# Optimization experiments

Measured on AMD Instinct MI355X. Metric: run time of the kernel, lower is better.

Reference implementation:

```python
import jax, jax.numpy as jnp
import numpy as np

N = 100000
E = 1600000
NUM_GRAPHS = 128
IN_C = 11
HID = 128


def setup_inputs() -> dict:
    key = jax.random.key(0)
    ks = jax.random.split(key, 16)
    x = jax.random.normal(ks[0], (N, IN_C), dtype=jnp.float32)
    edge_index = jax.random.randint(ks[1], (2, E), 0, N, dtype=jnp.int64)
    batch = jnp.sort(jax.random.randint(ks[2], (N,), 0, NUM_GRAPHS, dtype=jnp.int64))
    s_in = 1.0 / np.sqrt(IN_C)
    s_h = 1.0 / np.sqrt(HID)
    params = {
        'W1': jax.random.normal(ks[3], (IN_C, HID), jnp.float32) * s_in,
        'b1': jnp.zeros((HID,), jnp.float32),
        'W2': jax.random.normal(ks[4], (HID, HID), jnp.float32) * s_h,
        'b2': jnp.zeros((HID,), jnp.float32),
        'W4': jax.random.normal(ks[5], (HID, HID), jnp.float32) * s_h,
        'b4': jnp.zeros((HID,), jnp.float32),
        'Wd1': jax.random.normal(ks[6], (HID, HID), jnp.float32) * s_h,
        'bd1': jnp.zeros((HID,), jnp.float32),
        'Wd2': jax.random.normal(ks[7], (HID, HID), jnp.float32) * s_h,
        'bd2': jnp.zeros((HID,), jnp.float32),
        'Wo': jax.random.normal(ks[8], (HID, 1), jnp.float32) * s_h,
        'bo': jnp.zeros((1,), jnp.float32),
    }
    return {'x': x, 'edge_index': edge_index, 'batch': batch, **params}


def _gcn_norm(edge_index, n_nodes):
    # add self loops, compute symmetric normalization (PyG GCNConv defaults)
    loop = jnp.arange(n_nodes, dtype=edge_index.dtype)
    row = jnp.concatenate([edge_index[0], loop])
    col = jnp.concatenate([edge_index[1], loop])
    deg = jax.ops.segment_sum(jnp.ones_like(col, dtype=jnp.float32), col,
                              num_segments=n_nodes)
    dinv = jnp.where(deg > 0, jax.lax.rsqrt(deg), 0.0)
    norm = dinv[row] * dinv[col]  # [E+N]
    return row, col, norm


def _gcn_conv(h, row, col, norm, W, b, n_nodes):
    h = h @ W  # dense lin first (PyG order)
    msg = norm[:, None] * h[row]            # gather + normalize
    out = jax.ops.segment_sum(msg, col, num_segments=n_nodes)  # scatter-add
    return out + b


def reference(x, edge_index, batch, W1, b1, W2, b2, W4, b4,
              Wd1, bd1, Wd2, bd2, Wo, bo):
    n = x.shape[0]
    row, col, norm = _gcn_norm(edge_index, n)
    # dropout is identity in eval mode
    h = jax.nn.relu(_gcn_conv(x, row, col, norm, W1, b1, n))
    h = jax.nn.relu(_gcn_conv(h, row, col, norm, W2, b2, n))
    h = _gcn_conv(h, row, col, norm, W4, b4, n)
    # global_mean_pool over batch ids
    sums = jax.ops.segment_sum(h, batch, num_segments=NUM_GRAPHS)
    cnts = jax.ops.segment_sum(jnp.ones((n,), jnp.float32), batch,
                               num_segments=NUM_GRAPHS)
    g = sums / jnp.maximum(cnts, 1.0)[:, None]  # [NUM_GRAPHS, HID]
    g = jax.nn.relu(g @ Wd1 + bd1)
    g = jax.nn.relu(g @ Wd2 + bd2)
    return g @ Wo + bo  # [NUM_GRAPHS, 1]
```

## Files before the change

### kernel.cpp

```cpp
#include <hip/hip_runtime.h>
#include <hip/hip_fp16.h>

#define HIDDEN 128
#define BSHIFT 8
#define BMASK 255
#define CHUNK 4096
#define BCAP 6144

typedef _Float16 h8 __attribute__((ext_vector_type(8)));
typedef float f4x __attribute__((ext_vector_type(4)));

__global__ __launch_bounds__(256) void fill_bin(const int* __restrict__ row,
                                                const int* __restrict__ col,
                                                int* __restrict__ bcnt,
                                                int2* __restrict__ ptmp, int E) {
    __shared__ int cnt[512], start[512], place[512], gbase[512];
    __shared__ int ssum[256];
    __shared__ int2 stage[CHUNK];
    int t = threadIdx.x;
    int e0 = blockIdx.x * CHUNK;
    int e1 = min(e0 + CHUNK, E);
    cnt[t] = 0; cnt[t + 256] = 0;
    __syncthreads();
    for (int e = e0 + t; e < e1; e += 256)
        atomicAdd(&cnt[col[e] >> BSHIFT], 1);
    __syncthreads();
    int s2 = cnt[2 * t] + cnt[2 * t + 1];
    ssum[t] = s2;
    __syncthreads();
    for (int d = 1; d < 256; d <<= 1) {
        int v = (t >= d) ? ssum[t - d] : 0;
        __syncthreads();
        ssum[t] += v;
        __syncthreads();
    }
    int excl = ssum[t] - s2;
    start[2 * t] = excl;
    start[2 * t + 1] = excl + cnt[2 * t];
    place[2 * t] = excl;
    place[2 * t + 1] = excl + cnt[2 * t];
    __syncthreads();
    for (int e = e0 + t; e < e1; e += 256) {
        int c = col[e], r = row[e];
        int slot = atomicAdd(&place[c >> BSHIFT], 1);
        stage[slot] = make_int2(r, c);
    }
    {
        int c0 = cnt[t], c1 = cnt[t + 256];
        if (c0 > 0) gbase[t] = atomicAdd(&bcnt[t], c0);
        if (c1 > 0) gbase[t + 256] = atomicAdd(&bcnt[t + 256], c1);
    }
    __syncthreads();
    int n = e1 - e0;
    for (int i = t; i < n; i += 256) {
        int2 p = stage[i];
        int b = p.y >> BSHIFT;
        ptmp[(size_t)b * BCAP + gbase[b] + (i - start[b])] = p;
    }
}

__global__ __launch_bounds__(512) void scan_buckets(const int* __restrict__ bcnt,
                                                    int* __restrict__ bbase, int NB) {
    __shared__ int s[512];
    int t = threadIdx.x;
    int v0 = (t < NB) ? bcnt[t] : 0;
    s[t] = v0;
    __syncthreads();
    for (int d = 1; d < 512; d <<= 1) {
        int v = (t >= d) ? s[t - d] : 0;
        __syncthreads();
        s[t] += v;
        __syncthreads();
    }
    bbase[t] = s[t] - v0;
}

__global__ __launch_bounds__(256) void fill_scatter(const int2* __restrict__ ptmp,
                                                    const int* __restrict__ bcnt,
                                                    const int* __restrict__ bbase,
                                                    const float* __restrict__ x,
                                                    int* __restrict__ offsets,
                                                    float* __restrict__ dinv,
                                                    int* __restrict__ sorted_r,
                                                    __half* __restrict__ xp,
                                                    int N, int E) {
    __shared__ int2 stage[BCAP];
    __shared__ int cnt[256], loff[256], cur[256];
    int b = blockIdx.x, t = threadIdx.x;
    int m = bcnt[b];
    int base = bbase[b];
    int nbase = b << BSHIFT;
    cnt[t] = 0;
    __syncthreads();
    for (int i = t; i < m; i += 256) {
        int2 p = ptmp[(size_t)b * BCAP + i];
        stage[i] = p;
        atomicAdd(&cnt[p.y & BMASK], 1);
    }
    __syncthreads();
    int my = cnt[t];
    loff[t] = my;
    __syncthreads();
    for (int d = 1; d < 256; d <<= 1) {
        int v = (t >= d) ? loff[t - d] : 0;
        __syncthreads();
        loff[t] += v;
        __syncthreads();
    }
    int excl = loff[t] - my;
    cur[t] = excl;
    int node = nbase + t;
    float dv = rsqrtf((float)(my + 1));
    if (node < N) {
        offsets[node] = base + excl;
        dinv[node] = dv;
        __half hrow[16];
#pragma unroll
        for (int c = 0; c < 11; ++c)
            hrow[c] = __float2half(x[(size_t)node * 11 + c] * dv);
#pragma unroll
        for (int c = 11; c < 16; ++c) hrow[c] = __float2half(0.f);
        *(uint4*)(xp + (size_t)node * 16)     = *(uint4*)hrow;
        *(uint4*)(xp + (size_t)node * 16 + 8) = *(uint4*)(hrow + 8);
    }
    if (b == gridDim.x - 1 && t == 0) offsets[N] = E;
    __syncthreads();
    for (int i = t; i < m; i += 256) {
        int2 p = stage[i];
        int slot = atomicAdd(&cur[p.y & BMASK], 1);
        sorted_r[base + slot] = p.x;
    }
}

__global__ __launch_bounds__(256) void agg16_fused(const __half* __restrict__ xp,
                                                   const float* __restrict__ W1,
                                                   const int* __restrict__ offsets,
                                                   const int* __restrict__ sorted_r,
                                                   const float* __restrict__ dinv,
                                                   __half* __restrict__ out, int N) {
    __shared__ float W1s[11 * 128];
    __shared__ float arow[4][16];
    int t = threadIdx.x;
    for (int q = t; q < 11 * 128; q += 256) W1s[q] = W1[q];
    int wv = t >> 6, lane = t & 63;
    int c = blockIdx.x * 4 + wv;
    bool valid = c < N;
    int g = lane >> 3, cp = lane & 7;
    const __half2* xp2 = (const __half2*)xp;
    float ax = 0.f, ay = 0.f;
    if (valid) {
        int beg = offsets[c], end = offsets[c + 1];
        if (g == 0) {
            float2 v = __half22float2(xp2[(size_t)c * 8 + cp]);
            ax = v.x; ay = v.y;
        }
        int i = beg;
        for (; i + 16 <= end; i += 16) {
            int r0 = sorted_r[i + g];
            int r1 = sorted_r[i + g + 8];
            float2 v0 = __half22float2(xp2[(size_t)r0 * 8 + cp]);
            float2 v1 = __half22float2(xp2[(size_t)r1 * 8 + cp]);
            ax += v0.x + v1.x; ay += v0.y + v1.y;
        }
        if (i < end) {
            int last = end - 1;
            int i0 = i + g, i1 = i + g + 8;
            int r0 = sorted_r[min(i0, last)];
            int r1 = sorted_r[min(i1, last)];
            float2 v0 = __half22float2(xp2[(size_t)r0 * 8 + cp]);
            float2 v1 = __half22float2(xp2[(size_t)r1 * 8 + cp]);
            if (i0 <= last) { ax += v0.x; ay += v0.y; }
            if (i1 <= last) { ax += v1.x; ay += v1.y; }
        }
    }
    ax += __shfl_xor(ax, 32); ay += __shfl_xor(ay, 32);
    ax += __shfl_xor(ax, 16); ay += __shfl_xor(ay, 16);
    ax += __shfl_xor(ax, 8);  ay += __shfl_xor(ay, 8);
    if (valid && lane < 8) {
        float dc = dinv[c];
        arow[wv][cp * 2]     = ax * dc;
        arow[wv][cp * 2 + 1] = ay * dc;
    }
    __syncthreads();
    int j = t & 127, half = t >> 7;
#pragma unroll
    for (int nn = 0; nn < 2; ++nn) {
        int n = half * 2 + nn;
        int node = blockIdx.x * 4 + n;
        if (node < N) {
            float acc = 0.f;
#pragma unroll
            for (int cc = 0; cc < 11; ++cc) acc += arow[n][cc] * W1s[cc * 128 + j];
            out[(size_t)node * HIDDEN + j] = __float2half(acc);
        }
    }
}

__global__ __launch_bounds__(256) void pack_w(const float* __restrict__ W,
                                              const float* __restrict__ bias,
                                              __half* __restrict__ packed) {
    int q = blockIdx.x * 256 + threadIdx.x;
    if (q < 2048) {
        int s = q >> 9, rem = q & 511, ct = rem >> 6, l = rem & 63;
        int b = l >> 4, n = l & 15;
        __half hi8[8], lo8[8];
#pragma unroll
        for (int i = 0; i < 8; ++i) {
            float w = W[(s * 32 + b * 8 + i) * HIDDEN + ct * 16 + n];
            __half h = __float2half(w);
            hi8[i] = h;
            lo8[i] = __float2half(w - __half2float(h));
        }
        *(uint4*)(packed + (size_t)q * 8)         = *(uint4*)hi8;
        *(uint4*)(packed + 16384 + (size_t)q * 8) = *(uint4*)lo8;
    }
    if (q < 128) packed[32768 + q] = __float2half(bias[q]);
}

__global__ __launch_bounds__(256, 2) void gemm_mfma(const __half* __restrict__ H,
                                                    const __half* __restrict__ packed,
                                                    const float* __restrict__ dinv,
                                                    __half* __restrict__ out,
                                                    int N, int ngroups) {
    int l = threadIdx.x & 63, wv = threadIdx.x >> 6;
    int cthalf = wv & 1;
    int n16 = l & 15, koct = l >> 4;
    h8 whi[4][4], wlo[4][4];
#pragma unroll
    for (int s = 0; s < 4; ++s)
#pragma unroll
        for (int mt = 0; mt < 4; ++mt) {
            int ct = cthalf * 4 + mt;
            whi[s][mt] = *(const h8*)(packed + (size_t)((s * 8 + ct) * 64 + l) * 8);
            wlo[s][mt] = *(const h8*)(packed + 16384 + (size_t)((s * 8 + ct) * 64 + l) * 8);
        }
    h8 biasf[4];
    const __half* bias_h = packed + 32768;
#pragma unroll
    for (int s = 0; s < 4; ++s)
        biasf[s] = *(const h8*)(bias_h + s * 32 + koct * 8);

    for (int g = blockIdx.x * 2 + (wv >> 1); g < ngroups; g += gridDim.x * 2) {
        int node = g * 16 + n16;
        bool ok = node < N;
        f4x acc[4];
#pragma unroll
        for (int mt = 0; mt < 4; ++mt) acc[mt] = (f4x){0.f, 0.f, 0.f, 0.f};
#pragma unroll
        for (int s = 0; s < 4; ++s) {
            uint4 bv = make_uint4(0u, 0u, 0u, 0u);
            if (ok) bv = *(const uint4*)(H + (size_t)node * HIDDEN + s * 32 + koct * 8);
            __half2* bh2 = (__half2*)&bv;
            const __half2* bb = (const __half2*)&biasf[s];
#pragma unroll
            for (int p = 0; p < 4; ++p) {
                float2 f  = __half22float2(bh2[p]);
                float2 bf = __half22float2(bb[p]);
                bh2[p] = __floats2half2_rn(fmaxf(f.x + bf.x, 0.f), fmaxf(f.y + bf.y, 0.f));
            }
            h8 bfrag = *(h8*)&bv;
#pragma unroll
            for (int mt = 0; mt < 4; ++mt) {
                acc[mt] = __builtin_amdgcn_mfma_f32_16x16x32_f16(whi[s][mt], bfrag, acc[mt], 0, 0, 0);
                acc[mt] = __builtin_amdgcn_mfma_f32_16x16x32_f16(wlo[s][mt], bfrag, acc[mt], 0, 0, 0);
            }
        }
        if (ok) {
            float dv = dinv[node];
#pragma unroll
            for (int mt = 0; mt < 4; ++mt) {
                int ch = (cthalf * 4 + mt) * 16 + koct * 4;
                __half2 h01 = __floats2half2_rn(acc[mt][0] * dv, acc[mt][1] * dv);
                __half2 h23 = __floats2half2_rn(acc[mt][2] * dv, acc[mt][3] * dv);
                uint2 o;
                o.x = *(unsigned int*)&h01; o.y = *(unsigned int*)&h23;
                *(uint2*)(out + (size_t)node * HIDDEN + ch) = o;
            }
        }
    }
}

__global__ __launch_bounds__(256) void agg128h(const __half* __restrict__ src,
                                               __half* __restrict__ dst,
                                               const int* __restrict__ offsets,
                                               const int* __restrict__ sorted_r,
                                               const float* __restrict__ dinv, int N) {
    int wid  = (blockIdx.x * 256 + threadIdx.x) >> 6;
    int lane = threadIdx.x & 63;
    if (wid >= N) return;
    int c = wid;
    int beg = offsets[c], end = offsets[c + 1];
    int g = lane >> 4, sub = lane & 15;
    const uint4* hp = (const uint4*)src;
    float a0=0.f,a1=0.f,a2=0.f,a3=0.f,a4=0.f,a5=0.f,a6=0.f,a7=0.f;

    auto accum = [&](uint4 u) {
        __half2 p0 = *(__half2*)&u.x, p1 = *(__half2*)&u.y;
        __half2 p2 = *(__half2*)&u.z, p3 = *(__half2*)&u.w;
        float2 f0 = __half22float2(p0), f1 = __half22float2(p1);
        float2 f2 = __half22float2(p2), f3 = __half22float2(p3);
        a0 += f0.x; a1 += f0.y; a2 += f1.x; a3 += f1.y;
        a4 += f2.x; a5 += f2.y; a6 += f3.x; a7 += f3.y;
    };

    if (g == 0) accum(hp[(size_t)c * 16 + sub]);

    int i = beg;
    for (; i + 16 <= end; i += 16) {
        int base = i + 4 * g;
        int r0 = sorted_r[base + 0];
        int r1 = sorted_r[base + 1];
        int r2 = sorted_r[base + 2];
        int r3 = sorted_r[base + 3];
        uint4 u0 = hp[(size_t)r0 * 16 + sub];
        uint4 u1 = hp[(size_t)r1 * 16 + sub];
        uint4 u2 = hp[(size_t)r2 * 16 + sub];
        uint4 u3 = hp[(size_t)r3 * 16 + sub];
        accum(u0); accum(u1); accum(u2); accum(u3);
    }
    if (i < end) {
        int last = end - 1;
        int i0 = i + 4 * g, i1 = i0 + 1, i2 = i0 + 2, i3 = i0 + 3;
        int r0 = sorted_r[min(i0, last)];
        int r1 = sorted_r[min(i1, last)];
        int r2 = sorted_r[min(i2, last)];
        int r3 = sorted_r[min(i3, last)];
        uint4 u0 = hp[(size_t)r0 * 16 + sub];
        uint4 u1 = hp[(size_t)r1 * 16 + sub];
        uint4 u2 = hp[(size_t)r2 * 16 + sub];
        uint4 u3 = hp[(size_t)r3 * 16 + sub];
        if (i0 <= last) accum(u0);
        if (i1 <= last) accum(u1);
        if (i2 <= last) accum(u2);
        if (i3 <= last) accum(u3);
    }
    a0 += __shfl_xor(a0, 32); a1 += __shfl_xor(a1, 32);
    a2 += __shfl_xor(a2, 32); a3 += __shfl_xor(a3, 32);
    a4 += __shfl_xor(a4, 32); a5 += __shfl_xor(a5, 32);
    a6 += __shfl_xor(a6, 32); a7 += __shfl_xor(a7, 32);
    a0 += __shfl_xor(a0, 16); a1 += __shfl_xor(a1, 16);
    a2 += __shfl_xor(a2, 16); a3 += __shfl_xor(a3, 16);
    a4 += __shfl_xor(a4, 16); a5 += __shfl_xor(a5, 16);
    a6 += __shfl_xor(a6, 16); a7 += __shfl_xor(a7, 16);
    if (g == 0) {
        float dc = dinv[c];
        __half2 h01 = __floats2half2_rn(a0 * dc, a1 * dc);
        __half2 h23 = __floats2half2_rn(a2 * dc, a3 * dc);
        __half2 h45 = __floats2half2_rn(a4 * dc, a5 * dc);
        __half2 h67 = __floats2half2_rn(a6 * dc, a7 * dc);
        uint4 o;
        o.x = *(unsigned int*)&h01; o.y = *(unsigned int*)&h23;
        o.z = *(unsigned int*)&h45; o.w = *(unsigned int*)&h67;
        ((uint4*)dst)[(size_t)c * 16 + sub] = o;
    }
}

__global__ __launch_bounds__(256) void pool_partial(const __half* __restrict__ h,
                                                    const int* __restrict__ batch,
                                                    float* __restrict__ partials, int N) {
    int g = blockIdx.x >> 3, part8 = blockIdx.x & 7;
    int t = threadIdx.x, cp = t & 63, rp = t >> 6;
    int lo = 0, hi = N;
    while (lo < hi) { int m = (lo + hi) >> 1; if (batch[m] < g) lo = m + 1; else hi = m; }
    int beg = lo;
    lo = beg; hi = N;
    while (lo < hi) { int m = (lo + hi) >> 1; if (batch[m] < g + 1) lo = m + 1; else hi = m; }
    int end = lo;
    const __half2* h2 = (const __half2*)h;
    float ax = 0.f, ay = 0.f;
    for (int i = beg + part8 * 4 + rp; i < end; i += 32) {
        float2 v = __half22float2(h2[(size_t)i * 64 + cp]);
        ax += v.x; ay += v.y;
    }
    __shared__ float px[4][64], py[4][64];
    px[rp][cp] = ax; py[rp][cp] = ay;
    __syncthreads();
    if (rp == 0) {
        float sx = px[0][cp] + px[1][cp] + px[2][cp] + px[3][cp];
        float sy = py[0][cp] + py[1][cp] + py[2][cp] + py[3][cp];
        partials[(size_t)blockIdx.x * 128 + cp * 2]     = sx;
        partials[(size_t)blockIdx.x * 128 + cp * 2 + 1] = sy;
    }
}

__global__ __launch_bounds__(128) void head_kernel(const float* __restrict__ partials,
                                                   const int* __restrict__ batch,
                                                   const float* __restrict__ b4,
                                                   const float* __restrict__ Wd1,
                                                   const float* __restrict__ bd1,
                                                   const float* __restrict__ Wd2,
                                                   const float* __restrict__ bd2,
                                                   const float* __restrict__ Wo,
                                                   const float* __restrict__ bo,
                                                   float* __restrict__ out, int N) {
    int g = blockIdx.x;
    int j = threadIdx.x;
    __shared__ float sA[128], sB[128], red[128];
    int lo = 0, hi = N;
    while (lo < hi) { int m = (lo + hi) >> 1; if (batch[m] < g) lo = m + 1; else hi = m; }
    int beg = lo;
    lo = beg; hi = N;
    while (lo < hi) { int m = (lo + hi) >> 1; if (batch[m] < g + 1) lo = m + 1; else hi = m; }
    int cnt = lo - beg;
    float s = 0.f;
#pragma unroll
    for (int p = 0; p < 8; ++p) s += partials[(size_t)(g * 8 + p) * 128 + j];
    sA[j] = (cnt > 0) ? s / (float)cnt + b4[j] : 0.f;
    __syncthreads();
    float a = bd1[j];
#pragma unroll 4
    for (int k = 0; k < 128; ++k) a += sA[k] * Wd1[k * HIDDEN + j];
    sB[j] = fmaxf(a, 0.f);
    __syncthreads();
    a = bd2[j];
#pragma unroll 4
    for (int k = 0; k < 128; ++k) a += sB[k] * Wd2[k * HIDDEN + j];
    red[j] = fmaxf(a, 0.f) * Wo[j];
    __syncthreads();
    for (int d = 64; d > 0; d >>= 1) {
        if (j < d) red[j] += red[j + d];
        __syncthreads();
    }
    if (j == 0) out[g] = red[0] + bo[0];
}

extern "C" void kernel_launch(void* const* d_in, const int* in_sizes, int n_in,
                              void* d_out, int out_size, void* d_ws, size_t ws_size,
                              hipStream_t stream) {
    const float* x   = (const float*)d_in[0];
    const int*   ei  = (const int*)d_in[1];
    const int*   bat = (const int*)d_in[2];
    const float* W1  = (const float*)d_in[3];
    const float* b1  = (const float*)d_in[4];
    const float* W2  = (const float*)d_in[5];
    const float* b2  = (const float*)d_in[6];
    const float* W4  = (const float*)d_in[7];
    const float* b4  = (const float*)d_in[8];
    const float* Wd1 = (const float*)d_in[9];
    const float* bd1 = (const float*)d_in[10];
    const float* Wd2 = (const float*)d_in[11];
    const float* bd2 = (const float*)d_in[12];
    const float* Wo  = (const float*)d_in[13];
    const float* bo  = (const float*)d_in[14];
    float* out = (float*)d_out;

    const int N = in_sizes[0] / 11;
    const int E = in_sizes[1] / 2;
    const int* row = ei;
    const int* col = ei + E;
    const int B = (N + (1 << BSHIFT) - 1) >> BSHIFT;
    const int ngroups = (N + 15) / 16;

    size_t off = 0;
    auto carve = [&](size_t bytes) {
        void* p = (char*)d_ws + off;
        off += (bytes + 255) & ~(size_t)255;
        return p;
    };
    __half* bufHA    = (__half*)carve((size_t)N * HIDDEN * 2);
    __half* bufHB    = (__half*)carve((size_t)N * HIDDEN * 2);
    __half* xp       = (__half*)carve((size_t)N * 16 * 2);
    int*    offsets  = (int*)carve((size_t)(N + 1) * 4);
    float*  dinv     = (float*)carve((size_t)N * 4);
    int*    sorted_r = (int*)carve((size_t)E * 4);
    int*    bcnt     = (int*)carve((size_t)512 * 4);
    int*    bbase    = (int*)carve((size_t)512 * 4);
    float*  partials = (float*)carve((size_t)128 * 8 * 128 * 4);
    __half* packW2   = (__half*)carve((size_t)(32768 + 128) * 2);
    __half* packW4   = (__half*)carve((size_t)(32768 + 128) * 2);
    int2* ptmp = (int2*)bufHA;
    (void)ws_size; (void)n_in; (void)out_size;

    hipMemsetAsync(bcnt, 0, (size_t)512 * 4, stream);
    fill_bin<<<(E + CHUNK - 1) / CHUNK, 256, 0, stream>>>(row, col, bcnt, ptmp, E);
    scan_buckets<<<1, 512, 0, stream>>>(bcnt, bbase, B);
    fill_scatter<<<B, 256, 0, stream>>>(ptmp, bcnt, bbase, x, offsets, dinv,
                                        sorted_r, xp, N, E);

    pack_w<<<8, 256, 0, stream>>>(W2, b1, packW2);
    pack_w<<<8, 256, 0, stream>>>(W4, b2, packW4);

    int aggBlocks = (N + 3) / 4;

    agg16_fused<<<aggBlocks, 256, 0, stream>>>(xp, W1, offsets, sorted_r, dinv,
                                               bufHA, N);
    gemm_mfma<<<1024, 256, 0, stream>>>(bufHA, packW2, dinv, bufHB, N, ngroups);
    agg128h<<<aggBlocks, 256, 0, stream>>>(bufHB, bufHA, offsets, sorted_r, dinv, N);
    gemm_mfma<<<1024, 256, 0, stream>>>(bufHA, packW4, dinv, bufHB, N, ngroups);
    agg128h<<<aggBlocks, 256, 0, stream>>>(bufHB, bufHA, offsets, sorted_r, dinv, N);
    pool_partial<<<128 * 8, 256, 0, stream>>>(bufHA, bat, partials, N);
    head_kernel<<<128, 128, 0, stream>>>(partials, bat, b4, Wd1, bd1, Wd2, bd2,
                                         Wo, bo, out, N);
}
```

Baseline: 310.4 us.

## Store hidden features in channel-sliced layout and aggregate per 16-channel slice

Hidden activations are now stored as 8 slices of 16 channels each, laid out [slice][node][16], instead of row-major [node][128]. Aggregation launches 8x more blocks, each gathering one 32-byte slice per neighbor, so the working set of each slice (about 3.2 MB) can stay cache-resident across the random gathers. The GEMM, first-layer fused kernel and pooling are updated to read and write this layout. The cost is more blocks, repeated reads of offsets and indices per slice, and smaller 8-byte per-lane loads.

Result: slower. 597.8 us (+92.6%).

```diff
diff --git a/kernel.cpp b/kernel.cpp
--- a/kernel.cpp
+++ b/kernel.cpp
@@ -6,6 +6,7 @@
 #define BMASK 255
 #define CHUNK 4096
 #define BCAP 6144
+
 
 typedef _Float16 h8 __attribute__((ext_vector_type(8)));
 typedef float f4x __attribute__((ext_vector_type(4)));
@@ -191,7 +192,7 @@
             float acc = 0.f;
 #pragma unroll
             for (int cc = 0; cc < 11; ++cc) acc += arow[n][cc] * W1s[cc * 128 + j];
-            out[(size_t)node * HIDDEN + j] = __float2half(acc);
+            out[((size_t)(j >> 4) * N + node) * 16 + (j & 15)] = __float2half(acc);
         }
     }
 }
@@ -240,6 +241,8 @@
     for (int s = 0; s < 4; ++s)
         biasf[s] = *(const h8*)(bias_h + s * 32 + koct * 8);
 
+    int lsl = koct >> 1, lc0 = (koct & 1) * 8;
+
     for (int g = blockIdx.x * 2 + (wv >> 1); g < ngroups; g += gridDim.x * 2) {
         int node = g * 16 + n16;
         bool ok = node < N;
@@ -249,7 +252,10 @@
 #pragma unroll
         for (int s = 0; s < 4; ++s) {
             uint4 bv = make_uint4(0u, 0u, 0u, 0u);
-            if (ok) bv = *(const uint4*)(H + (size_t)node * HIDDEN + s * 32 + koct * 8);
+            if (ok) {
+                int sl = 2 * s + lsl;
+                bv = *(const uint4*)(H + ((size_t)sl * N + node) * 16 + lc0);
+            }
             __half2* bh2 = (__half2*)&bv;
             const __half2* bb = (const __half2*)&biasf[s];
 #pragma unroll
@@ -269,89 +275,64 @@
             float dv = dinv[node];
 #pragma unroll
             for (int mt = 0; mt < 4; ++mt) {
-                int ch = (cthalf * 4 + mt) * 16 + koct * 4;
+                int sl = cthalf * 4 + mt;
                 __half2 h01 = __floats2half2_rn(acc[mt][0] * dv, acc[mt][1] * dv);
                 __half2 h23 = __floats2half2_rn(acc[mt][2] * dv, acc[mt][3] * dv);
                 uint2 o;
                 o.x = *(unsigned int*)&h01; o.y = *(unsigned int*)&h23;
-                *(uint2*)(out + (size_t)node * HIDDEN + ch) = o;
+                *(uint2*)(out + ((size_t)sl * N + node) * 16 + koct * 4) = o;
             }
         }
     }
 }
 
-__global__ __launch_bounds__(256) void agg128h(const __half* __restrict__ src,
-                                               __half* __restrict__ dst,
-                                               const int* __restrict__ offsets,
-                                               const int* __restrict__ sorted_r,
-                                               const float* __restrict__ dinv, int N) {
-    int wid  = (blockIdx.x * 256 + threadIdx.x) >> 6;
+__global__ __launch_bounds__(256) void agg128h_sliced(const __half* __restrict__ src,
+                                                      __half* __restrict__ dst,
+                                                      const int* __restrict__ offsets,
+                                                      const int* __restrict__ sorted_r,
+                                                      const float* __restrict__ dinv,
+                                                      int N) {
+    int s = blockIdx.x & 7;
+    int c = (blockIdx.x >> 3) * 4 + (threadIdx.x >> 6);
     int lane = threadIdx.x & 63;
-    if (wid >= N) return;
-    int c = wid;
+    if (c >= N) return;
+    int g = lane >> 2, sub = lane & 3;
     int beg = offsets[c], end = offsets[c + 1];
-    int g = lane >> 4, sub = lane & 15;
-    const uint4* hp = (const uint4*)src;
-    float a0=0.f,a1=0.f,a2=0.f,a3=0.f,a4=0.f,a5=0.f,a6=0.f,a7=0.f;
-
-    auto accum = [&](uint4 u) {
-        __half2 p0 = *(__half2*)&u.x, p1 = *(__half2*)&u.y;
-        __half2 p2 = *(__half2*)&u.z, p3 = *(__half2*)&u.w;
-        float2 f0 = __half22float2(p0), f1 = __half22float2(p1);
-        float2 f2 = __half22float2(p2), f3 = __half22float2(p3);
+    const uint2* sp = (const uint2*)src + (size_t)s * N * 4;
+    float a0 = 0.f, a1 = 0.f, a2 = 0.f, a3 = 0.f;
+    auto accum = [&](uint2 u) {
+        float2 f0 = __half22float2(*(__half2*)&u.x);
+        float2 f1 = __half22float2(*(__half2*)&u.y);
         a0 += f0.x; a1 += f0.y; a2 += f1.x; a3 += f1.y;
-        a4 += f2.x; a5 += f2.y; a6 += f3.x; a7 += f3.y;
     };
-
-    if (g == 0) accum(hp[(size_t)c * 16 + sub]);
-
+    if (g == 0) accum(sp[(size_t)c * 4 + sub]);
     int i = beg;
     for (; i + 16 <= end; i += 16) {
-        int base = i + 4 * g;
-        int r0 = sorted_r[base + 0];
-        int r1 = sorted_r[base + 1];
-        int r2 = sorted_r[base + 2];
-        int r3 = sorted_r[base + 3];
-        uint4 u0 = hp[(size_t)r0 * 16 + sub];
-        uint4 u1 = hp[(size_t)r1 * 16 + sub];
-        uint4 u2 = hp[(size_t)r2 * 16 + sub];
-        uint4 u3 = hp[(size_t)r3 * 16 + sub];
-        accum(u0); accum(u1); accum(u2); accum(u3);
+        int r = sorted_r[i + g];
+        accum(sp[(size_t)r * 4 + sub]);
     }
     if (i < end) {
         int last = end - 1;
-        int i0 = i + 4 * g, i1 = i0 + 1, i2 = i0 + 2, i3 = i0 + 3;
-        int r0 = sorted_r[min(i0, last)];
-        int r1 = sorted_r[min(i1, last)];
-        int r2 = sorted_r[min(i2, last)];
-        int r3 = sorted_r[min(i3, last)];
-        uint4 u0 = hp[(size_t)r0 * 16 + sub];
-        uint4 u1 = hp[(size_t)r1 * 16 + sub];
-        uint4 u2 = hp[(size_t)r2 * 16 + sub];
-        uint4 u3 = hp[(size_t)r3 * 16 + sub];
-        if (i0 <= last) accum(u0);
-        if (i1 <= last) accum(u1);
-        if (i2 <= last) accum(u2);
-        if (i3 <= last) accum(u3);
+        int ii = i + g;
+        int r = sorted_r[min(ii, last)];
+        uint2 u = sp[(size_t)r * 4 + sub];
+        if (ii <= last) accum(u);
     }
     a0 += __shfl_xor(a0, 32); a1 += __shfl_xor(a1, 32);
     a2 += __shfl_xor(a2, 32); a3 += __shfl_xor(a3, 32);
-    a4 += __shfl_xor(a4, 32); a5 += __shfl_xor(a5, 32);
-    a6 += __shfl_xor(a6, 32); a7 += __shfl_xor(a7, 32);
     a0 += __shfl_xor(a0, 16); a1 += __shfl_xor(a1, 16);
     a2 += __shfl_xor(a2, 16); a3 += __shfl_xor(a3, 16);
-    a4 += __shfl_xor(a4, 16); a5 += __shfl_xor(a5, 16);
-    a6 += __shfl_xor(a6, 16); a7 += __shfl_xor(a7, 16);
+    a0 += __shfl_xor(a0, 8);  a1 += __shfl_xor(a1, 8);
+    a2 += __shfl_xor(a2, 8);  a3 += __shfl_xor(a3, 8);
+    a0 += __shfl_xor(a0, 4);  a1 += __shfl_xor(a1, 4);
+    a2 += __shfl_xor(a2, 4);  a3 += __shfl_xor(a3, 4);
     if (g == 0) {
         float dc = dinv[c];
         __half2 h01 = __floats2half2_rn(a0 * dc, a1 * dc);
         __half2 h23 = __floats2half2_rn(a2 * dc, a3 * dc);
-        __half2 h45 = __floats2half2_rn(a4 * dc, a5 * dc);
-        __half2 h67 = __floats2half2_rn(a6 * dc, a7 * dc);
-        uint4 o;
+        uint2 o;
         o.x = *(unsigned int*)&h01; o.y = *(unsigned int*)&h23;
-        o.z = *(unsigned int*)&h45; o.w = *(unsigned int*)&h67;
-        ((uint4*)dst)[(size_t)c * 16 + sub] = o;
+        ((uint2*)dst + (size_t)s * N * 4)[(size_t)c * 4 + sub] = o;
     }
 }
 
@@ -367,9 +348,11 @@
     while (lo < hi) { int m = (lo + hi) >> 1; if (batch[m] < g + 1) lo = m + 1; else hi = m; }
     int end = lo;
     const __half2* h2 = (const __half2*)h;
+    size_t sbase = (size_t)(cp >> 3) * N * 8;
+    int soff = cp & 7;
     float ax = 0.f, ay = 0.f;
     for (int i = beg + part8 * 4 + rp; i < end; i += 32) {
-        float2 v = __half22float2(h2[(size_t)i * 64 + cp]);
+        float2 v = __half22float2(h2[sbase + (size_t)i * 8 + soff]);
         ax += v.x; ay += v.y;
     }
     __shared__ float px[4][64], py[4][64];
@@ -480,14 +463,17 @@
     pack_w<<<8, 256, 0, stream>>>(W2, b1, packW2);
     pack_w<<<8, 256, 0, stream>>>(W4, b2, packW4);
 
-    int aggBlocks = (N + 3) / 4;
+    int aggBlocks   = (N + 3) / 4;
+    int aggSliced   = 8 * ((N + 3) / 4);
 
     agg16_fused<<<aggBlocks, 256, 0, stream>>>(xp, W1, offsets, sorted_r, dinv,
                                                bufHA, N);
     gemm_mfma<<<1024, 256, 0, stream>>>(bufHA, packW2, dinv, bufHB, N, ngroups);
-    agg128h<<<aggBlocks, 256, 0, stream>>>(bufHB, bufHA, offsets, sorted_r, dinv, N);
+    agg128h_sliced<<<aggSliced, 256, 0, stream>>>(bufHB, bufHA, offsets, sorted_r,
+                                                  dinv, N);
     gemm_mfma<<<1024, 256, 0, stream>>>(bufHA, packW4, dinv, bufHB, N, ngroups);
-    agg128h<<<aggBlocks, 256, 0, stream>>>(bufHB, bufHA, offsets, sorted_r, dinv, N);
+    agg128h_sliced<<<aggSliced, 256, 0, stream>>>(bufHB, bufHA, offsets, sorted_r,
+                                                  dinv, N);
     pool_partial<<<128 * 8, 256, 0, stream>>>(bufHA, bat, partials, N);
     head_kernel<<<128, 128, 0, stream>>>(partials, bat, b4, Wd1, bd1, Wd2, bd2,
                                          Wo, bo, out, N);
```
